# Performance work log

Measured on AMD Instinct MI355X. Metric: run time of the kernel, lower is better.

Reference implementation:

```python
import jax, jax.numpy as jnp
import numpy as np
from jax import lax

B, S, D, STEPS, OUT = 512, 256, 256, 256, 3


def setup_inputs() -> dict:
    key = jax.random.key(0)
    ks = jax.random.split(key, 16)
    sc = 0.05
    n = lambda k, shp: jax.random.normal(k, shp, jnp.float32) * sc
    return {
        "e_all": jax.random.normal(ks[0], (B, S, D), jnp.float32),
        "e_last": jax.random.normal(ks[1], (1, B, D), jnp.float32),
        # NN_Attention params
        "Wa": n(ks[2], (D, D)), "ba": n(ks[3], (D,)),
        "Ua": n(ks[4], (D, D)), "bu": n(ks[5], (D,)),
        "Va": n(ks[6], (D,)), "bv": n(ks[7], ()),
        # GRU params (PyTorch layout: W_ih [3D, 3+D], W_hh [3D, D])
        "W_ih": n(ks[8], (3 * D, D + 3)), "b_ih": n(ks[9], (3 * D,)),
        "W_hh": n(ks[10], (3 * D, D)), "b_hh": n(ks[11], (3 * D,)),
        # output linear D -> 3
        "Wo": n(ks[12], (OUT, D)), "bo": n(ks[13], (OUT,)),
    }


def _decode(e_all, e_last, Wa, ba, Ua, bu, Va, bv, W_ih, b_ih, W_hh, b_hh, Wo, bo):
    # Ua(keys) is constant across steps -> precompute once (same math)
    Ua_keys = jnp.einsum('bsd,ed->bse', e_all, Ua) + bu  # [B, S, D]

    def step(carry, _):
        h, x_in = carry
        # Bahdanau attention: Va(tanh(Wa(q) + Ua(keys)))
        q = h @ Wa.T + ba                                       # [B, D]
        scores = jnp.einsum('bsd,d->bs', jnp.tanh(q[:, None, :] + Ua_keys), Va) + bv
        w = jax.nn.softmax(scores, axis=-1)                     # [B, S]
        ctx = jnp.einsum('bs,bsd->bd', w, e_all)                # [B, D]
        # GRU cell on input [context ; d_input] (cat order matches torch code)
        x = jnp.concatenate([ctx, x_in], axis=-1)               # [B, D+3]
        gi = x @ W_ih.T + b_ih
        gh = h @ W_hh.T + b_hh
        i_r, i_z, i_n = jnp.split(gi, 3, axis=-1)
        h_r, h_z, h_n = jnp.split(gh, 3, axis=-1)
        r = jax.nn.sigmoid(i_r + h_r)
        z = jax.nn.sigmoid(i_z + h_z)
        nn_ = jnp.tanh(i_n + r * h_n)
        h_new = (1.0 - z) * nn_ + z * h
        out = h_new @ Wo.T + bo                                 # [B, 3]
        return (h_new, out), (out, w)

    h0 = e_last[0]                                              # [B, D]
    x0 = jnp.zeros((h0.shape[0], OUT), h0.dtype)
    (hT, _), (outs, ws) = lax.scan(step, (h0, x0), None, length=STEPS)
    d_outputs = outs.transpose(1, 0, 2)                         # [B, STEPS, 3]
    cross_attn = ws.transpose(1, 0, 2).reshape(h0.shape[0], 1, STEPS * S)
    return d_outputs, hT[None], cross_attn


def reference(e_all, e_last, Wa, ba, Ua, bu, Va, bv, W_ih, b_ih, W_hh, b_hh, Wo, bo):
    return _decode(e_all, e_last, Wa, ba, Ua, bu, Va, bv, W_ih, b_ih, W_hh, b_hh, Wo, bo)
```

## Files before the change

### kernel.cpp

```cpp
#include <hip/hip_runtime.h>
#include <hip/hip_bf16.h>
#include <stdint.h>

#define NB 512
#define NS 256
#define ND 256
#define NT 256
#define NO 3

#define LOG2E 1.44269504088896340736f
#define C2 (2.0f*LOG2E)

typedef float f32x2 __attribute__((ext_vector_type(2)));

#if __has_builtin(__builtin_amdgcn_exp2f)
__device__ __forceinline__ float exp2_fast(float x){ return __builtin_amdgcn_exp2f(x); }
#else
__device__ __forceinline__ float exp2_fast(float x){ return exp2f(x); }
#endif
#if __has_builtin(__builtin_amdgcn_rcpf)
__device__ __forceinline__ float rcp_fast(float x){ return __builtin_amdgcn_rcpf(x); }
#else
__device__ __forceinline__ float rcp_fast(float x){ return 1.0f/x; }
#endif

__device__ __forceinline__ float tanh_f(float x){
  float e = exp2_fast(x * C2);
  return 1.0f - 2.0f*rcp_fast(e + 1.0f);
}
__device__ __forceinline__ float sigm_f(float x){
  return rcp_fast(1.0f + exp2_fast(-x*LOG2E));
}
__device__ __forceinline__ float bflo(uint32_t u){ return __uint_as_float(u<<16); }
__device__ __forceinline__ float bfhi(uint32_t u){ return __uint_as_float(u & 0xffff0000u); }
__device__ __forceinline__ uint16_t f2bf(float f){
  uint32_t u = __float_as_uint(f);
  return (uint16_t)((u + 0x7fffu + ((u>>16)&1u)) >> 16);
}
__device__ __forceinline__ uint32_t pack2(float a, float b){
  return (uint32_t)f2bf(a) | ((uint32_t)f2bf(b) << 16);
}

#if __has_builtin(__builtin_amdgcn_fdot2_f32_bf16)
typedef __bf16 bfp2 __attribute__((ext_vector_type(2)));
__device__ __forceinline__ float dot2bf(uint32_t a, uint32_t b, float c){
  return __builtin_amdgcn_fdot2_f32_bf16(__builtin_bit_cast(bfp2, a),
                                         __builtin_bit_cast(bfp2, b), c, false);
}
#else
__device__ __forceinline__ float dot2bf(uint32_t a, uint32_t b, float c){
  return c + bflo(a)*bflo(b) + bfhi(a)*bfhi(b);
}
#endif

__device__ __forceinline__ uint8_t enc_e4m3(float x){
  uint32_t sign = (__float_as_uint(x) >> 31) << 7;
  float y = fminf(fabsf(x), 448.0f);
  uint32_t u = __float_as_uint(y);
  int e = (int)(u >> 23) - 127;
  uint32_t code;
  if (e < -6){
    code = (uint32_t)__float2int_rn(y * 512.0f);
  } else {
    uint32_t r = u + 0x000FFFFFu + ((u >> 20) & 1u);
    e = (int)(r >> 23) - 127;
    code = (uint32_t)((e + 7) << 3) | ((r >> 20) & 7u);
    if (code > 0x7Eu) code = 0x7Eu;
  }
  return (uint8_t)(sign | code);
}

#if __has_builtin(__builtin_amdgcn_cvt_pk_f32_fp8)
template<bool HI>
__device__ __forceinline__ f32x2 cvtpk_fp8(uint32_t w){
  return __builtin_amdgcn_cvt_pk_f32_fp8((int)w, HI);
}
#else
__device__ __forceinline__ float dec1_e4m3(uint32_t b){
  uint32_t s = (b >> 7) << 31;
  uint32_t em = b & 0x7fu;
  float mag;
  if (em >= 8u){
    mag = __uint_as_float((((em >> 3) + 120u) << 23) | ((em & 7u) << 20));
  } else {
    mag = (float)em * 0.001953125f;
  }
  return __uint_as_float(s | __float_as_uint(mag));
}
template<bool HI>
__device__ __forceinline__ f32x2 cvtpk_fp8(uint32_t w){
  uint32_t p = HI ? (w >> 16) : (w & 0xffffu);
  f32x2 r; r.x = dec1_e4m3(p & 0xffu); r.y = dec1_e4m3(p >> 8); return r;
}
#endif

__device__ __forceinline__ float s_dword(uint32_t dwv, float4 qq, float4 vv, float acc){
  f32x2 lo = cvtpk_fp8<false>(dwv);
  f32x2 hi = cvtpk_fp8<true>(dwv);
  float r;
  r = rcp_fast(exp2_fast(lo.x + qq.x) + 1.f); acc = fmaf(vv.x, r, acc);
  r = rcp_fast(exp2_fast(lo.y + qq.y) + 1.f); acc = fmaf(vv.y, r, acc);
  r = rcp_fast(exp2_fast(hi.x + qq.z) + 1.f); acc = fmaf(vv.z, r, acc);
  r = rcp_fast(exp2_fast(hi.y + qq.w) + 1.f); acc = fmaf(vv.w, r, acc);
  return acc;
}
__device__ __forceinline__ float c_dword(uint32_t dwv, float4 w4, float acc){
  f32x2 lo = cvtpk_fp8<false>(dwv);
  f32x2 hi = cvtpk_fp8<true>(dwv);
  return fmaf(w4.x,lo.x, fmaf(w4.y,lo.y, fmaf(w4.z,hi.x, fmaf(w4.w,hi.y, acc))));
}


__global__ void k_transpose(const float* __restrict__ src, float* __restrict__ dst,
                            int R, int C){
  int idx = blockIdx.x*256 + threadIdx.x;
  if (idx < R*C){
    int r = idx / C, c = idx - r*C;
    dst[c*R + r] = src[idx];
  }
}

__global__ void __launch_bounds__(256) k_uk(const float* __restrict__ e_all,
    const float* __restrict__ UaT, const float* __restrict__ bu,
    uint8_t* __restrict__ UKQ){
  __shared__ float At[ND][20];
  const int t = threadIdx.x;
  const int m0 = blockIdx.x * 16;
  const int b  = m0 >> 8;
  const int s0 = m0 & (NS-1);
  #pragma unroll
  for (int i=0;i<16;i++)
    At[t][i] = e_all[(size_t)(m0+i)*ND + t];
  __syncthreads();
  float acc[16];
  float bue = bu[t];
  #pragma unroll
  for (int i=0;i<16;i++) acc[i] = bue;
  for (int d=0; d<ND; ++d){
    float u = UaT[d*ND + t];
    const float4 a0 = *(const float4*)&At[d][0];
    const float4 a1 = *(const float4*)&At[d][4];
    const float4 a2 = *(const float4*)&At[d][8];
    const float4 a3 = *(const float4*)&At[d][12];
    acc[0]+=a0.x*u;  acc[1]+=a0.y*u;  acc[2]+=a0.z*u;  acc[3]+=a0.w*u;
    acc[4]+=a1.x*u;  acc[5]+=a1.y*u;  acc[6]+=a1.z*u;  acc[7]+=a1.w*u;
    acc[8]+=a2.x*u;  acc[9]+=a2.y*u;  acc[10]+=a2.z*u; acc[11]+=a2.w*u;
    acc[12]+=a3.x*u; acc[13]+=a3.y*u; acc[14]+=a3.z*u; acc[15]+=a3.w*u;
  }
  const int e16 = t>>4, j = t&15;
  uint8_t* base = UKQ + (((size_t)b*16 + e16)*256 + s0)*16 + j;
  #pragma unroll
  for (int i=0;i<16;i++){
    uint32_t mine = enc_e4m3(acc[i] * C2);
    uint32_t other = (uint32_t)__shfl_xor((int)mine, 1);
    if (!(t & 1))
      *(uint16_t*)(base + (size_t)i*16) = (uint16_t)(mine | (other << 8));
  }
}

__global__ void k_epq(const float* __restrict__ e_all, uint32_t* __restrict__ EPQ){
  int idx = blockIdx.x*256 + threadIdx.x;
  if (idx >= NB*64*256) return;
  int d  = idx & 255;
  int s4 = (idx >> 8) & 63;
  int b  = idx >> 14;
  const float* e = e_all + ((size_t)b*NS + 4*s4)*ND + d;
  uint32_t v = (uint32_t)enc_e4m3(e[0])
             | ((uint32_t)enc_e4m3(e[ND])   << 8)
             | ((uint32_t)enc_e4m3(e[2*ND]) << 16)
             | ((uint32_t)enc_e4m3(e[3*ND]) << 24);
  EPQ[idx] = v;
}

__global__ void k_pkq(const float* __restrict__ W_ih, const float* __restrict__ W_hh,
                      uint32_t* __restrict__ PKq){
  int idx = blockIdx.x*256 + threadIdx.x;
  if (idx >= 260*3*256) return;
  int d  = idx & 255;
  int gk = idx >> 8;
  int k2 = gk/3, g = gk - 3*k2;
  int col = g*256 + d;
  float w0 = 0.f, w1 = 0.f;
  if (k2 < 130){
    int k0 = 2*k2, k1 = k0+1;
    w0 = W_ih[(size_t)col*259 + k0];
    w1 = (k1 < 259) ? W_ih[(size_t)col*259 + k1] : 0.f;
  } else if (k2 < 258){
    int kk = 2*(k2-130);
    w0 = W_hh[(size_t)col*256 + kk];
    w1 = W_hh[(size_t)col*256 + kk+1];
  }
  PKq[idx] = pack2(w0, w1);
}

__global__ void k_pack_q(const float* __restrict__ Wa, uint32_t* __restrict__ PQ){
  int idx = blockIdx.x*256 + threadIdx.x;
  if (idx >= 128*256) return;
  int d = idx & 255, k2 = idx >> 8;
  PQ[idx] = pack2(Wa[(size_t)d*256 + 2*k2], Wa[(size_t)d*256 + 2*k2 + 1]);
}

__global__ void __launch_bounds__(1024, 4) k_decode(
    const uint8_t* __restrict__ UKQ, const uint32_t* __restrict__ EPQ,
    const uint32_t* __restrict__ PKq, const uint32_t* __restrict__ PQ,
    const float* __restrict__ e_last,
    const float* __restrict__ Va, const float* __restrict__ bv,
    const float* __restrict__ b_ih, const float* __restrict__ b_hh,
    const float* __restrict__ ba, const float* __restrict__ bo,
    const float* __restrict__ Wo,
    float* __restrict__ dout, float* __restrict__ hT_out, float* __restrict__ ca)
{
  __shared__ __align__(16) uint8_t  ukl[65536];
  __shared__ __align__(16) uint32_t epl[16384];
  __shared__ __align__(16) float    scr[16][ND];
  __shared__ float    hf[ND];
  __shared__ float    xin[4];
  __shared__ uint32_t xb[260];
  __shared__ __align__(16) float qL[ND];
  __shared__ __align__(16) float va2[ND];
  __shared__ float    WoL[3*ND];
  __shared__ __align__(16) float wl[NS];
  __shared__ float    red[8];

  const int t    = threadIdx.x;
  const int d    = t & 255;
  const int q4   = t >> 8;
  const int lane = t & 63;
  const int w    = t >> 6;
  const int b0   = blockIdx.x * 2;

  if (q4 == 0){
    va2[d] = 2.0f*Va[d];
    WoL[d] = Wo[d]; WoL[256+d] = Wo[256+d]; WoL[512+d] = Wo[512+d];
  }
  const float bias_r  = b_ih[d]     + b_hh[d];
  const float bias_z  = b_ih[256+d] + b_hh[256+d];
  const float bias_ni = b_ih[512+d];
  const float bias_nh = b_hh[512+d];
  const float ba_d = ba[d];
  const float bv0  = bv[0];
  const float bo0 = bo[0], bo1 = bo[1], bo2 = bo[2];
  __syncthreads();
  float sumVaQ = 0.f;
  {
    #pragma unroll 8
    for (int e = q4*64; e < q4*64+64; ++e) sumVaQ += va2[e];
    sumVaQ *= 0.5f;
  }

  #pragma unroll 1
  for (int r=0; r<2; ++r){
    const int b = b0 + r;

    {
      const uint4* srcU = (const uint4*)(UKQ + (size_t)b*65536);
      uint4* dstU = (uint4*)ukl;
      #pragma unroll
      for (int i=0;i<4;i++) dstU[t + i*1024] = srcU[t + i*1024];
      const uint4* srcE = (const uint4*)(EPQ + (size_t)b*16384);
      uint4* dstE = (uint4*)epl;
      #pragma unroll
      for (int i=0;i<4;i++) dstE[t + i*1024] = srcE[t + i*1024];
    }
    if (q4 == 0){
      hf[d] = e_last[(size_t)b*ND + d];
      if (d < 4) xin[d] = 0.f;
    }
    __syncthreads();
    if (t < 128) xb[130+t] = pack2(hf[2*t], hf[2*t+1]);
    if (t == 128){ xb[128]=0u; xb[129]=0u; xb[258]=0u; xb[259]=0u; }
    __syncthreads();

    float* ca_b = ca   + (size_t)b*(NT*NS);
    float* do_b = dout + (size_t)b*(NT*NO);

    #pragma unroll 1
    for (int step=0; step<NT; ++step){
      {
        float aq = 0.f;
        const uint32_t* pq = PQ + (size_t)(q4*32)*256 + d;
        const uint32_t* xh = &xb[130 + q4*32];
        #pragma unroll 1
        for (int kk=0; kk<32; kk+=8){
          uint32_t wv[8], xv[8];
          #pragma unroll
          for (int j=0;j<8;j++){ wv[j] = pq[(kk+j)*256]; xv[j] = xh[kk+j]; }
          #pragma unroll
          for (int j=0;j<8;j++) aq = dot2bf(wv[j], xv[j], aq);
        }
        scr[q4][d] = aq;
      }
      __syncthreads();
      if (q4 == 0)
        qL[d] = ((scr[0][d]+scr[1][d]) + (scr[2][d]+scr[3][d]) + ba_d) * C2;
      __syncthreads();

      {
        float acc = 0.f;
        #pragma unroll
        for (int j=0;j<4;j++){
          uint4 u = *(const uint4*)(ukl + (size_t)(q4*4+j)*4096 + d*16);
          const float* qb = &qL[q4*64 + j*16];
          const float* vb = &va2[q4*64 + j*16];
          acc = s_dword(u.x, *(const float4*)&qb[0],  *(const float4*)&vb[0],  acc);
          acc = s_dword(u.y, *(const float4*)&qb[4],  *(const float4*)&vb[4],  acc);
          acc = s_dword(u.z, *(const float4*)&qb[8],  *(const float4*)&vb[8],  acc);
          acc = s_dword(u.w, *(const float4*)&qb[12], *(const float4*)&vb[12], acc);
        }
        scr[q4][d] = sumVaQ - acc;
      }
      __syncthreads();

      float p_reg = 0.f;
      if (q4 == 0){
        float sc = (scr[0][d]+scr[1][d]) + (scr[2][d]+scr[3][d]) + bv0;
        p_reg = exp2_fast(sc * LOG2E);
        float ssum = p_reg;
        #pragma unroll
        for (int o=32;o;o>>=1) ssum += __shfl_xor(ssum, o);
        if (lane==0) red[w] = ssum;
      }
      __syncthreads();
      if (q4 == 0){
        float ssum = (red[0]+red[1]) + (red[2]+red[3]);
        float wgt = p_reg * rcp_fast(ssum);
        __builtin_nontemporal_store(wgt, &ca_b[(size_t)step*NS + d]);
        wl[d] = wgt;
      }
      __syncthreads();

      {
        float c0=0,c1=0,c2=0,c3=0;
        #pragma unroll
        for (int i=0;i<4;i++){
          int s4 = w*4 + i;
          uint4 ev = *(const uint4*)(epl + (size_t)s4*256 + lane*4);
          float4 w4 = *(const float4*)&wl[s4*4];
          c0 = c_dword(ev.x, w4, c0);
          c1 = c_dword(ev.y, w4, c1);
          c2 = c_dword(ev.z, w4, c2);
          c3 = c_dword(ev.w, w4, c3);
        }
        *(float4*)&scr[w][lane*4] = make_float4(c0,c1,c2,c3);
      }
      __syncthreads();
      if (q4 == 0){
        float cx = 0.f;
        #pragma unroll
        for (int i=0;i<16;i++) cx += scr[i][d];
        float other = __shfl_xor(cx, 1);
        if (!(d&1)) xb[d>>1] = pack2(cx, other);
        if (d==128) xb[128] = pack2(xin[0], xin[1]);
        if (d==129) xb[129] = pack2(xin[2], 0.f);
      }
      __syncthreads();

      {
        float ar=0.f, az=0.f, an=0.f;
        const int k0 = q4*65;
        const uint32_t* pk = PKq + (size_t)k0*768 + d;
        #pragma unroll 1
        for (int g=0; g<64; g+=8){
          uint32_t wr[8], wz[8], wn[8], xv[8];
          #pragma unroll
          for (int j=0;j<8;j++){
            const uint32_t* p = pk + (size_t)(g+j)*768;
            wr[j]=p[0]; wz[j]=p[256]; wn[j]=p[512];
            xv[j]=xb[k0+g+j];
          }
          #pragma unroll
          for (int j=0;j<8;j++){
            ar=dot2bf(wr[j],xv[j],ar); az=dot2bf(wz[j],xv[j],az); an=dot2bf(wn[j],xv[j],an);
          }
        }
        {
          const uint32_t* p = pk + (size_t)64*768;
          uint32_t xa = xb[k0+64];
          ar=dot2bf(p[0],xa,ar); az=dot2bf(p[256],xa,az); an=dot2bf(p[512],xa,an);
        }
        scr[q4*3+0][d]=ar; scr[q4*3+1][d]=az; scr[q4*3+2][d]=an;
      }
      __syncthreads();
      if (q4 == 0){
        float ar  = (scr[0][d]+scr[3][d]) + (scr[6][d]+scr[9][d]) + bias_r;
        float az  = (scr[1][d]+scr[4][d]) + (scr[7][d]+scr[10][d]) + bias_z;
        float ani =  scr[2][d]+scr[5][d]  + bias_ni;
        float anh =  scr[8][d]+scr[11][d] + bias_nh;
        float rg = sigm_f(ar);
        float zg = sigm_f(az);
        float ng = tanh_f(ani + rg*anh);
        float hnew = (1.f-zg)*ng + zg*hf[d];
        hf[d] = hnew;
        float other = __shfl_xor(hnew, 1);
        if (!(d&1)) xb[130 + (d>>1)] = pack2(hnew, other);
      }
      __syncthreads();

      if (w == 0){
        float p0=0,p1=0,p2=0;
        #pragma unroll
        for (int i=0;i<4;i++){
          float hv = hf[i*64 + lane];
          p0 = fmaf(hv, WoL[      i*64+lane], p0);
          p1 = fmaf(hv, WoL[256 + i*64+lane], p1);
          p2 = fmaf(hv, WoL[512 + i*64+lane], p2);
        }
        #pragma unroll
        for (int o=32;o;o>>=1){
          p0+=__shfl_xor(p0,o); p1+=__shfl_xor(p1,o); p2+=__shfl_xor(p2,o);
        }
        if (lane==0){
          float o0=p0+bo0, o1=p1+bo1, o2=p2+bo2;
          __builtin_nontemporal_store(o0, &do_b[(size_t)step*NO+0]);
          __builtin_nontemporal_store(o1, &do_b[(size_t)step*NO+1]);
          __builtin_nontemporal_store(o2, &do_b[(size_t)step*NO+2]);
          xin[0]=o0; xin[1]=o1; xin[2]=o2;
        }
      }
    }

    __syncthreads();
    if (q4 == 0) hT_out[(size_t)b*ND + d] = hf[d];
    __syncthreads();
  }
}


extern "C" void kernel_launch(void* const* d_in, const int* in_sizes, int n_in,
                              void* d_out, int out_size, void* d_ws, size_t ws_size,
                              hipStream_t stream) {
  const float* e_all  = (const float*)d_in[0];
  const float* e_last = (const float*)d_in[1];
  const float* Wa     = (const float*)d_in[2];
  const float* ba     = (const float*)d_in[3];
  const float* Ua     = (const float*)d_in[4];
  const float* bu     = (const float*)d_in[5];
  const float* Va     = (const float*)d_in[6];
  const float* bv     = (const float*)d_in[7];
  const float* W_ih   = (const float*)d_in[8];
  const float* b_ih   = (const float*)d_in[9];
  const float* W_hh   = (const float*)d_in[10];
  const float* b_hh   = (const float*)d_in[11];
  const float* Wo     = (const float*)d_in[12];
  const float* bo     = (const float*)d_in[13];

  char* ws = (char*)d_ws;
  uint8_t*  UKQ = (uint8_t*) (ws + 0ull);
  uint32_t* EPQ = (uint32_t*)(ws + 33554432ull);
  uint32_t* PKq = (uint32_t*)(ws + 67108864ull);
  uint32_t* PQ  = (uint32_t*)(ws + 67907584ull);
  float*    UaT = (float*)   (ws + 68038656ull);

  float* dout = (float*)d_out;
  float* hT   = dout + (size_t)NB*NT*NO;
  float* ca   = hT   + (size_t)NB*ND;

  k_transpose<<<(ND*ND+255)/256,256,0,stream>>>(Ua, UaT, ND, ND);
  k_uk<<<NB*NS/16,256,0,stream>>>(e_all, UaT, bu, UKQ);
  k_epq<<<(NB*64*256+255)/256,256,0,stream>>>(e_all, EPQ);
  k_pkq<<<(260*3*256+255)/256,256,0,stream>>>(W_ih, W_hh, PKq);
  k_pack_q<<<(128*256+255)/256,256,0,stream>>>(Wa, PQ);

  k_decode<<<NB/2,1024,0,stream>>>(UKQ, EPQ, PKq, PQ, e_last, Va, bv,
                                   b_ih, b_hh, ba, bo, Wo, dout, hT, ca);
}
```

Baseline: 6.861 ms.

## Fuse hidden-state W_hh GEMV into the query projection pass

Packs Wa and the three W_hh gate rows into one uint4 per element so the h-dependent query projection and all hidden-side GRU gate products are computed in a single pass at the start of each step. The later GRU pass now covers only the W_ih input part, halving its K range, with weights interleaved r/z/n for contiguous loads. This moves work off the critical path after the context reduction and cuts per-step weight loads, at the cost of more registers and a new shared buffer for partial gate sums.

```diff
diff --git a/kernel.cpp b/kernel.cpp
--- a/kernel.cpp
+++ b/kernel.cpp
@@ -172,37 +172,43 @@
   EPQ[idx] = v;
 }
 
-__global__ void k_pkq(const float* __restrict__ W_ih, const float* __restrict__ W_hh,
-                      uint32_t* __restrict__ PKq){
-  int idx = blockIdx.x*256 + threadIdx.x;
-  if (idx >= 260*3*256) return;
-  int d  = idx & 255;
-  int gk = idx >> 8;
-  int k2 = gk/3, g = gk - 3*k2;
-  int col = g*256 + d;
-  float w0 = 0.f, w1 = 0.f;
-  if (k2 < 130){
-    int k0 = 2*k2, k1 = k0+1;
-    w0 = W_ih[(size_t)col*259 + k0];
-    w1 = (k1 < 259) ? W_ih[(size_t)col*259 + k1] : 0.f;
-  } else if (k2 < 258){
-    int kk = 2*(k2-130);
-    w0 = W_hh[(size_t)col*256 + kk];
-    w1 = W_hh[(size_t)col*256 + kk+1];
-  }
-  PKq[idx] = pack2(w0, w1);
-}
-
-__global__ void k_pack_q(const float* __restrict__ Wa, uint32_t* __restrict__ PQ){
+__global__ void k_wh(const float* __restrict__ Wa, const float* __restrict__ W_hh,
+                     uint4* __restrict__ WH){
   int idx = blockIdx.x*256 + threadIdx.x;
   if (idx >= 128*256) return;
   int d = idx & 255, k2 = idx >> 8;
-  PQ[idx] = pack2(Wa[(size_t)d*256 + 2*k2], Wa[(size_t)d*256 + 2*k2 + 1]);
+  uint4 v;
+  v.x = pack2(Wa  [(size_t)d*256       + 2*k2], Wa  [(size_t)d*256       + 2*k2+1]);
+  v.y = pack2(W_hh[(size_t)d*256       + 2*k2], W_hh[(size_t)d*256       + 2*k2+1]);
+  v.z = pack2(W_hh[(size_t)(256+d)*256 + 2*k2], W_hh[(size_t)(256+d)*256 + 2*k2+1]);
+  v.w = pack2(W_hh[(size_t)(512+d)*256 + 2*k2], W_hh[(size_t)(512+d)*256 + 2*k2+1]);
+  WH[idx] = v;
+}
+
+__global__ void k_wx(const float* __restrict__ W_ih, uint32_t* __restrict__ WX){
+  int idx = blockIdx.x*256 + threadIdx.x;
+  if (idx >= 132*256) return;
+  int d = idx & 255, k2 = idx >> 8;
+  float r0=0,r1=0,z0=0,z1=0,n0=0,n1=0;
+  int ka = 2*k2, kb = 2*k2+1;
+  if (ka < 259){
+    r0 = W_ih[(size_t)d*259       + ka];
+    z0 = W_ih[(size_t)(256+d)*259 + ka];
+    n0 = W_ih[(size_t)(512+d)*259 + ka];
+  }
+  if (kb < 259){
+    r1 = W_ih[(size_t)d*259       + kb];
+    z1 = W_ih[(size_t)(256+d)*259 + kb];
+    n1 = W_ih[(size_t)(512+d)*259 + kb];
+  }
+  WX[(size_t)idx*3+0] = pack2(r0,r1);
+  WX[(size_t)idx*3+1] = pack2(z0,z1);
+  WX[(size_t)idx*3+2] = pack2(n0,n1);
 }
 
 __global__ void __launch_bounds__(1024, 4) k_decode(
     const uint8_t* __restrict__ UKQ, const uint32_t* __restrict__ EPQ,
-    const uint32_t* __restrict__ PKq, const uint32_t* __restrict__ PQ,
+    const uint4* __restrict__ WH, const uint32_t* __restrict__ WX,
     const float* __restrict__ e_last,
     const float* __restrict__ Va, const float* __restrict__ bv,
     const float* __restrict__ b_ih, const float* __restrict__ b_hh,
@@ -213,6 +219,7 @@
   __shared__ __align__(16) uint8_t  ukl[65536];
   __shared__ __align__(16) uint32_t epl[16384];
   __shared__ __align__(16) float    scr[16][ND];
+  __shared__ float    ghp[3][ND];
   __shared__ float    hf[ND];
   __shared__ float    xin[4];
   __shared__ uint32_t xb[260];
@@ -277,22 +284,30 @@
     #pragma unroll 1
     for (int step=0; step<NT; ++step){
       {
-        float aq = 0.f;
-        const uint32_t* pq = PQ + (size_t)(q4*32)*256 + d;
+        float aq=0.f, ar=0.f, az=0.f, an=0.f;
+        const uint4* wh = WH + (size_t)(q4*32)*256 + d;
         const uint32_t* xh = &xb[130 + q4*32];
         #pragma unroll 1
-        for (int kk=0; kk<32; kk+=8){
-          uint32_t wv[8], xv[8];
-          #pragma unroll
-          for (int j=0;j<8;j++){ wv[j] = pq[(kk+j)*256]; xv[j] = xh[kk+j]; }
-          #pragma unroll
-          for (int j=0;j<8;j++) aq = dot2bf(wv[j], xv[j], aq);
-        }
-        scr[q4][d] = aq;
-      }
-      __syncthreads();
-      if (q4 == 0)
-        qL[d] = ((scr[0][d]+scr[1][d]) + (scr[2][d]+scr[3][d]) + ba_d) * C2;
+        for (int kk=0; kk<32; kk+=4){
+          uint4 w0 = wh[(size_t)(kk+0)*256];
+          uint4 w1 = wh[(size_t)(kk+1)*256];
+          uint4 w2 = wh[(size_t)(kk+2)*256];
+          uint4 w3 = wh[(size_t)(kk+3)*256];
+          uint32_t x0 = xh[kk+0], x1 = xh[kk+1], x2 = xh[kk+2], x3 = xh[kk+3];
+          aq=dot2bf(w0.x,x0,aq); ar=dot2bf(w0.y,x0,ar); az=dot2bf(w0.z,x0,az); an=dot2bf(w0.w,x0,an);
+          aq=dot2bf(w1.x,x1,aq); ar=dot2bf(w1.y,x1,ar); az=dot2bf(w1.z,x1,az); an=dot2bf(w1.w,x1,an);
+          aq=dot2bf(w2.x,x2,aq); ar=dot2bf(w2.y,x2,ar); az=dot2bf(w2.z,x2,az); an=dot2bf(w2.w,x2,an);
+          aq=dot2bf(w3.x,x3,aq); ar=dot2bf(w3.y,x3,ar); az=dot2bf(w3.z,x3,az); an=dot2bf(w3.w,x3,an);
+        }
+        scr[q4*4+0][d]=aq; scr[q4*4+1][d]=ar; scr[q4*4+2][d]=az; scr[q4*4+3][d]=an;
+      }
+      __syncthreads();
+      if (q4 == 0){
+        qL[d]     = ((scr[0][d]+scr[4][d]) + (scr[8][d]+scr[12][d]) + ba_d) * C2;
+        ghp[0][d] =  (scr[1][d]+scr[5][d]) + (scr[9][d]+scr[13][d]);
+        ghp[1][d] =  (scr[2][d]+scr[6][d]) + (scr[10][d]+scr[14][d]);
+        ghp[2][d] =  (scr[3][d]+scr[7][d]) + (scr[11][d]+scr[15][d]);
+      }
       __syncthreads();
 
       {
@@ -357,35 +372,38 @@
 
       {
         float ar=0.f, az=0.f, an=0.f;
-        const int k0 = q4*65;
-        const uint32_t* pk = PKq + (size_t)k0*768 + d;
+        const int k0 = q4*33;
+        const uint32_t* wx = WX + ((size_t)k0*256 + d)*3;
         #pragma unroll 1
-        for (int g=0; g<64; g+=8){
-          uint32_t wr[8], wz[8], wn[8], xv[8];
-          #pragma unroll
-          for (int j=0;j<8;j++){
-            const uint32_t* p = pk + (size_t)(g+j)*768;
-            wr[j]=p[0]; wz[j]=p[256]; wn[j]=p[512];
-            xv[j]=xb[k0+g+j];
-          }
-          #pragma unroll
-          for (int j=0;j<8;j++){
-            ar=dot2bf(wr[j],xv[j],ar); az=dot2bf(wz[j],xv[j],az); an=dot2bf(wn[j],xv[j],an);
-          }
+        for (int kk=0; kk<32; kk+=4){
+          const uint32_t* p0 = wx + (size_t)(kk+0)*768;
+          const uint32_t* p1 = wx + (size_t)(kk+1)*768;
+          const uint32_t* p2 = wx + (size_t)(kk+2)*768;
+          const uint32_t* p3 = wx + (size_t)(kk+3)*768;
+          uint32_t r0=p0[0], z0=p0[1], n0=p0[2];
+          uint32_t r1=p1[0], z1=p1[1], n1=p1[2];
+          uint32_t r2=p2[0], z2=p2[1], n2=p2[2];
+          uint32_t r3=p3[0], z3=p3[1], n3=p3[2];
+          uint32_t x0 = xb[k0+kk+0], x1 = xb[k0+kk+1];
+          uint32_t x2 = xb[k0+kk+2], x3 = xb[k0+kk+3];
+          ar=dot2bf(r0,x0,ar); az=dot2bf(z0,x0,az); an=dot2bf(n0,x0,an);
+          ar=dot2bf(r1,x1,ar); az=dot2bf(z1,x1,az); an=dot2bf(n1,x1,an);
+          ar=dot2bf(r2,x2,ar); az=dot2bf(z2,x2,az); an=dot2bf(n2,x2,an);
+          ar=dot2bf(r3,x3,ar); az=dot2bf(z3,x3,az); an=dot2bf(n3,x3,an);
         }
         {
-          const uint32_t* p = pk + (size_t)64*768;
-          uint32_t xa = xb[k0+64];
-          ar=dot2bf(p[0],xa,ar); az=dot2bf(p[256],xa,az); an=dot2bf(p[512],xa,an);
+          const uint32_t* p = wx + (size_t)32*768;
+          uint32_t xa = xb[k0+32];
+          ar=dot2bf(p[0],xa,ar); az=dot2bf(p[1],xa,az); an=dot2bf(p[2],xa,an);
         }
         scr[q4*3+0][d]=ar; scr[q4*3+1][d]=az; scr[q4*3+2][d]=an;
       }
       __syncthreads();
       if (q4 == 0){
-        float ar  = (scr[0][d]+scr[3][d]) + (scr[6][d]+scr[9][d]) + bias_r;
-        float az  = (scr[1][d]+scr[4][d]) + (scr[7][d]+scr[10][d]) + bias_z;
-        float ani =  scr[2][d]+scr[5][d]  + bias_ni;
-        float anh =  scr[8][d]+scr[11][d] + bias_nh;
+        float ar  = (scr[0][d]+scr[3][d]) + (scr[6][d]+scr[9][d])  + ghp[0][d] + bias_r;
+        float az  = (scr[1][d]+scr[4][d]) + (scr[7][d]+scr[10][d]) + ghp[1][d] + bias_z;
+        float ani = (scr[2][d]+scr[5][d]) + (scr[8][d]+scr[11][d]) + bias_ni;
+        float anh = ghp[2][d] + bias_nh;
         float rg = sigm_f(ar);
         float zg = sigm_f(az);
         float ng = tanh_f(ani + rg*anh);
@@ -447,8 +465,8 @@
   char* ws = (char*)d_ws;
   uint8_t*  UKQ = (uint8_t*) (ws + 0ull);
   uint32_t* EPQ = (uint32_t*)(ws + 33554432ull);
-  uint32_t* PKq = (uint32_t*)(ws + 67108864ull);
-  uint32_t* PQ  = (uint32_t*)(ws + 67907584ull);
+  uint4*    WH  = (uint4*)   (ws + 67108864ull);
+  uint32_t* WX  = (uint32_t*)(ws + 67633152ull);
   float*    UaT = (float*)   (ws + 68038656ull);
 
   float* dout = (float*)d_out;
@@ -458,9 +476,9 @@
   k_transpose<<<(ND*ND+255)/256,256,0,stream>>>(Ua, UaT, ND, ND);
   k_uk<<<NB*NS/16,256,0,stream>>>(e_all, UaT, bu, UKQ);
   k_epq<<<(NB*64*256+255)/256,256,0,stream>>>(e_all, EPQ);
-  k_pkq<<<(260*3*256+255)/256,256,0,stream>>>(W_ih, W_hh, PKq);
-  k_pack_q<<<(128*256+255)/256,256,0,stream>>>(Wa, PQ);
-
-  k_decode<<<NB/2,1024,0,stream>>>(UKQ, EPQ, PKq, PQ, e_last, Va, bv,
+  k_wh<<<(128*256+255)/256,256,0,stream>>>(Wa, W_hh, WH);
+  k_wx<<<(132*256+255)/256,256,0,stream>>>(W_ih, WX);
+
+  k_decode<<<NB/2,1024,0,stream>>>(UKQ, EPQ, WH, WX, e_last, Va, bv,
                                    b_ih, b_hh, ba, bo, Wo, dout, hT, ca);
 }
```

After: 7.282 ms. 6.1% more time.
